# Optimization experiments

Measured on AMD Instinct MI355X. Metric: run time of the kernel, lower is better.

## Reference

```python
import jax, jax.numpy as jnp
import numpy as np

# model constants (from par)
DT = 0.05
TAU_M = 10.0
ALPHA = 1.0 - DT / TAU_M   # membrane leak factor
V_TH = 1.0                 # spike threshold
T, B, N = 500, 1024, 256


def setup_inputs() -> dict:
    key = jax.random.key(0)
    kx, kw = jax.random.split(key)
    x = jax.random.normal(kx, (T, B, N), dtype=jnp.float32)
    w = jax.random.normal(kw, (N,), dtype=jnp.float32) / np.sqrt(N).astype(np.float32)
    return {"x": x, "w": w}


def reference(x, w):
    """LIF neuron dynamics over T timesteps.

    Per step (matching NeuronClass_nn.__call__):
      v <- alpha * v + x_t @ w - v_th * stop_gradient(z)
      z <- 1[v - v_th > 0]
    Returns (v_seq, z_seq), each [T, B].
    """
    batch = x.shape[1]
    v0 = jnp.zeros((batch,), dtype=x.dtype)
    z0 = jnp.zeros((batch,), dtype=x.dtype)

    def step(carry, x_t):
        v, z = carry
        v = ALPHA * v + x_t @ w - V_TH * jax.lax.stop_gradient(z)
        z = (v - V_TH > 0).astype(v.dtype)
        return (v, z), (v, z)

    _, (v_seq, z_seq) = jax.lax.scan(step, (v0, z0), x)
    return v_seq, z_seq
```

## Files before the change

kernel.cpp:

```cpp
#include <hip/hip_runtime.h>


#define T_STEPS 500
#define BATCH   1024
#define NDIM    256
#define ALPHA_F 0.995f
#define TSTRIDE ((size_t)BATCH * NDIM)
#define DEPTH   16

__global__ __launch_bounds__(256) void lif_fused_kernel(
    const float* __restrict__ x, const float* __restrict__ w,
    float* __restrict__ vout, float* __restrict__ zout)
{
    const int wave = threadIdx.x >> 6;
    const int lane = threadIdx.x & 63;
    const int c    = blockIdx.x * 4 + wave;

    const float4 wv = *(const float4*)(w + lane * 4);
    const float* xbase = x + (size_t)c * NDIM + lane * 4;

    float v = 0.0f, z = 0.0f;

    auto step = [&](const float4 xv, const int t) {
        float p = xv.x * wv.x + xv.y * wv.y + xv.z * wv.z + xv.w * wv.w;
        p += __shfl_xor(p, 32, 64);
        p += __shfl_xor(p, 16, 64);
        p += __shfl_xor(p, 8, 64);
        p += __shfl_xor(p, 4, 64);
        p += __shfl_xor(p, 2, 64);
        p += __shfl_xor(p, 1, 64);
        v = ALPHA_F * v + p - z;
        z = (v - 1.0f > 0.0f) ? 1.0f : 0.0f;
        const size_t o = (size_t)t * BATCH + c;
        if (lane == 0) vout[o] = v;
        if (lane == 1) zout[o] = z;
    };

    float4 buf[DEPTH];
#pragma unroll
    for (int j = 0; j < DEPTH; ++j)
        buf[j] = *(const float4*)(xbase + (size_t)j * TSTRIDE);

    for (int t0 = 0; t0 < T_STEPS - 2 * DEPTH + 12; t0 += DEPTH) {
#pragma unroll
        for (int j = 0; j < DEPTH; ++j) {
            const int t = t0 + j;
            const float4 xv = buf[j];
            buf[j] = *(const float4*)(xbase + (size_t)(t + DEPTH) * TSTRIDE);
            step(xv, t);
        }
    }

    float4 buf2[4];
#pragma unroll
    for (int j = 0; j < 4; ++j)
        buf2[j] = *(const float4*)(xbase + (size_t)(496 + j) * TSTRIDE);
#pragma unroll
    for (int j = 0; j < DEPTH; ++j)
        step(buf[j], 480 + j);
#pragma unroll
    for (int j = 0; j < 4; ++j)
        step(buf2[j], 496 + j);
}

extern "C" void kernel_launch(void* const* d_in, const int* in_sizes, int n_in,
                              void* d_out, int out_size, void* d_ws, size_t ws_size,
                              hipStream_t stream)
{
    const float* x = (const float*)d_in[0];
    const float* w = (const float*)d_in[1];
    float* out  = (float*)d_out;
    float* vout = out;
    float* zout = out + (size_t)T_STEPS * BATCH;

    lif_fused_kernel<<<BATCH / 4, 256, 0, stream>>>(x, w, vout, zout);
}
```

Before: 677.8 us.

## Split LIF into parallel matvec kernel and lightweight sequential scan kernel

Replaces the single fused kernel, where each wave walked all timesteps serially, with two kernels. A bandwidth-oriented matvec kernel computes every x_t·w projection in parallel across all timesteps into a workspace buffer. A second kernel then runs the cheap recurrence per batch element, one thread per column, with software prefetch. This trades an extra write and read of the projection buffer and a second launch for full-device parallelism on the dominant memory read.

Result: no change. 688.8 us (+1.6%).

```diff
diff --git a/kernel.cpp b/kernel.cpp
--- a/kernel.cpp
+++ b/kernel.cpp
@@ -5,62 +5,79 @@
 #define BATCH   1024
 #define NDIM    256
 #define ALPHA_F 0.995f
-#define TSTRIDE ((size_t)BATCH * NDIM)
-#define DEPTH   16
+#define ROWS    (T_STEPS * BATCH)
+#define NGROUPS (ROWS / 4)
 
-__global__ __launch_bounds__(256) void lif_fused_kernel(
+__global__ __launch_bounds__(256) void lif_matvec_kernel(
     const float* __restrict__ x, const float* __restrict__ w,
-    float* __restrict__ vout, float* __restrict__ zout)
+    float* __restrict__ p)
 {
-    const int wave = threadIdx.x >> 6;
     const int lane = threadIdx.x & 63;
-    const int c    = blockIdx.x * 4 + wave;
+    const int wid  = (int)((blockIdx.x * blockDim.x + threadIdx.x) >> 6);
+    const int nw   = (int)((gridDim.x * blockDim.x) >> 6);
 
     const float4 wv = *(const float4*)(w + lane * 4);
-    const float* xbase = x + (size_t)c * NDIM + lane * 4;
+
+    for (int g = wid; g < NGROUPS; g += nw) {
+        const float* xr = x + (size_t)g * (4 * NDIM) + lane * 4;
+        const float4 a0 = *(const float4*)(xr);
+        const float4 a1 = *(const float4*)(xr + NDIM);
+        const float4 a2 = *(const float4*)(xr + 2 * NDIM);
+        const float4 a3 = *(const float4*)(xr + 3 * NDIM);
+
+        float s0 = a0.x * wv.x + a0.y * wv.y + a0.z * wv.z + a0.w * wv.w;
+        float s1 = a1.x * wv.x + a1.y * wv.y + a1.z * wv.z + a1.w * wv.w;
+        float s2 = a2.x * wv.x + a2.y * wv.y + a2.z * wv.z + a2.w * wv.w;
+        float s3 = a3.x * wv.x + a3.y * wv.y + a3.z * wv.z + a3.w * wv.w;
+
+#pragma unroll
+        for (int m = 32; m >= 1; m >>= 1) {
+            s0 += __shfl_xor(s0, m, 64);
+            s1 += __shfl_xor(s1, m, 64);
+            s2 += __shfl_xor(s2, m, 64);
+            s3 += __shfl_xor(s3, m, 64);
+        }
+
+        if (lane == 0)
+            *(float4*)(p + (size_t)g * 4) = make_float4(s0, s1, s2, s3);
+    }
+}
+
+#define DEPTH2 25
+
+__global__ __launch_bounds__(256) void lif_scan_kernel(
+    const float* p, float* vout, float* zout)
+{
+    const int c = blockIdx.x * 256 + threadIdx.x;
 
     float v = 0.0f, z = 0.0f;
+    float buf[DEPTH2];
+#pragma unroll
+    for (int j = 0; j < DEPTH2; ++j)
+        buf[j] = p[(size_t)j * BATCH + c];
 
-    auto step = [&](const float4 xv, const int t) {
-        float p = xv.x * wv.x + xv.y * wv.y + xv.z * wv.z + xv.w * wv.w;
-        p += __shfl_xor(p, 32, 64);
-        p += __shfl_xor(p, 16, 64);
-        p += __shfl_xor(p, 8, 64);
-        p += __shfl_xor(p, 4, 64);
-        p += __shfl_xor(p, 2, 64);
-        p += __shfl_xor(p, 1, 64);
-        v = ALPHA_F * v + p - z;
-        z = (v - 1.0f > 0.0f) ? 1.0f : 0.0f;
-        const size_t o = (size_t)t * BATCH + c;
-        if (lane == 0) vout[o] = v;
-        if (lane == 1) zout[o] = z;
-    };
-
-    float4 buf[DEPTH];
+    for (int t0 = 0; t0 < T_STEPS - DEPTH2; t0 += DEPTH2) {
 #pragma unroll
-    for (int j = 0; j < DEPTH; ++j)
-        buf[j] = *(const float4*)(xbase + (size_t)j * TSTRIDE);
-
-    for (int t0 = 0; t0 < T_STEPS - 2 * DEPTH + 12; t0 += DEPTH) {
-#pragma unroll
-        for (int j = 0; j < DEPTH; ++j) {
+        for (int j = 0; j < DEPTH2; ++j) {
             const int t = t0 + j;
-            const float4 xv = buf[j];
-            buf[j] = *(const float4*)(xbase + (size_t)(t + DEPTH) * TSTRIDE);
-            step(xv, t);
+            const float pt = buf[j];
+            buf[j] = p[(size_t)(t + DEPTH2) * BATCH + c];
+            v = ALPHA_F * v + pt - z;
+            z = (v - 1.0f > 0.0f) ? 1.0f : 0.0f;
+            vout[(size_t)t * BATCH + c] = v;
+            zout[(size_t)t * BATCH + c] = z;
         }
     }
 
-    float4 buf2[4];
 #pragma unroll
-    for (int j = 0; j < 4; ++j)
-        buf2[j] = *(const float4*)(xbase + (size_t)(496 + j) * TSTRIDE);
-#pragma unroll
-    for (int j = 0; j < DEPTH; ++j)
-        step(buf[j], 480 + j);
-#pragma unroll
-    for (int j = 0; j < 4; ++j)
-        step(buf2[j], 496 + j);
+    for (int j = 0; j < DEPTH2; ++j) {
+        const int t = T_STEPS - DEPTH2 + j;
+        const float pt = buf[j];
+        v = ALPHA_F * v + pt - z;
+        z = (v - 1.0f > 0.0f) ? 1.0f : 0.0f;
+        vout[(size_t)t * BATCH + c] = v;
+        zout[(size_t)t * BATCH + c] = z;
+    }
 }
 
 extern "C" void kernel_launch(void* const* d_in, const int* in_sizes, int n_in,
@@ -73,5 +90,8 @@
     float* vout = out;
     float* zout = out + (size_t)T_STEPS * BATCH;
 
-    lif_fused_kernel<<<BATCH / 4, 256, 0, stream>>>(x, w, vout, zout);
+    float* p = (ws_size >= (size_t)ROWS * sizeof(float)) ? (float*)d_ws : vout;
+
+    lif_matvec_kernel<<<2048, 256, 0, stream>>>(x, w, p);
+    lif_scan_kernel<<<BATCH / 256, 256, 0, stream>>>(p, vout, zout);
 }
```
